# Optimization experiments

Hardware: AMD Instinct MI355X
Metric: run time of the kernel (lower is better)

## Reference

```python
import jax, jax.numpy as jnp
import numpy as np

INPUT_DIM = 1024
HIDDEN_DIM = 128
TEMPERATURE = 1.0
TOPK = 10  # hard-coded k in the original forward


def setup_inputs() -> dict:
    key = jax.random.key(0)
    ks = jax.random.split(key, 7)
    B, N = 8, 50000
    s_in = 1.0 / np.sqrt(INPUT_DIM)
    s_h = 1.0 / np.sqrt(HIDDEN_DIM)
    return {
        "x": jax.random.normal(ks[0], (B, N, INPUT_DIM), dtype=jnp.float32),
        # torch Linear weight is [out,in]; we store transposed [in,out] for x @ W
        "Wv": jax.random.uniform(ks[1], (INPUT_DIM, HIDDEN_DIM), jnp.float32, -s_in, s_in),
        "bv": jax.random.uniform(ks[2], (HIDDEN_DIM,), jnp.float32, -s_in, s_in),
        "Wu": jax.random.uniform(ks[3], (INPUT_DIM, HIDDEN_DIM), jnp.float32, -s_in, s_in),
        "bu": jax.random.uniform(ks[4], (HIDDEN_DIM,), jnp.float32, -s_in, s_in),
        "Ww": jax.random.uniform(ks[5], (HIDDEN_DIM, 1), jnp.float32, -s_h, s_h),
        "bw": jax.random.uniform(ks[6], (1,), jnp.float32, -s_h, s_h),
    }


def reference(x, Wv, bv, Wu, bu, Ww, bw):
    # x: [B, N, D]. Dropout is identity in eval mode.
    def per_bag(xi):  # xi: [N, D]
        A_V = jnp.tanh(xi @ Wv + bv)              # [N, H]
        A_U = jax.nn.sigmoid(xi @ Wu + bu)        # [N, H] (gated attention)
        A = A_V * A_U
        scores = ((A @ Ww) + bw)[:, 0] / TEMPERATURE  # [N]
        _, top_idx = jax.lax.top_k(scores, TOPK)
        _, tail_idx = jax.lax.top_k(-scores, TOPK)
        idx = jnp.concatenate([top_idx, tail_idx])     # [2k]
        w = jax.nn.softmax(scores[idx])                # softmax over truncated set
        Z = w @ xi[idx]                                # [D]
        # dense analogue of the per-instance attention list (None -> 0)
        atten = jnp.zeros_like(scores).at[idx].set(w)  # [N]
        return Z, atten

    Z, atten = jax.vmap(per_bag)(x)  # Z: [B, D], atten: [B, N]
    return Z, atten
```

## Files before the change

kernel.cpp:

```cpp
#include <hip/hip_runtime.h>
#include <math.h>
#include <float.h>

#define INPUT_DIM 1024
#define HIDDEN 128
#define KSEL 10
#define KC 12

#define BM 64
#define BK 64
#define KT (INPUT_DIM / BK)
#define STH 512
#define NSEL1 32

typedef short short8 __attribute__((ext_vector_type(8)));
typedef float f32x4 __attribute__((ext_vector_type(4)));

static __device__ __forceinline__ unsigned short f2bf(float f) {
    union { float f; unsigned u; } v; v.f = f;
    unsigned r = v.u + 0x7FFF + ((v.u >> 16) & 1);
    return (unsigned short)(r >> 16);
}
static __device__ __forceinline__ float fast_tanh(float a) {
    float e = __expf(2.0f * a);
    return 1.0f - 2.0f / (e + 1.0f);
}
static __device__ __forceinline__ float fast_sigmoid(float a) {
    return 1.0f / (1.0f + __expf(-a));
}

__global__ __launch_bounds__(64) void repack_kernel(
    const float* __restrict__ Wv, const float* __restrict__ Wu,
    unsigned short* __restrict__ wp_hi)
{
    int bid = blockIdx.x;
    int l = threadIdx.x;
    int pc = (bid & 15) * 16 + (l & 15);
    int h = pc >> 1;
    const float* src = (pc & 1) ? Wu : Wv;
    int kbase = (bid >> 4) * 32 + (l >> 4) * 8;
    size_t off = ((size_t)bid * 64 + l) * 8;
    #pragma unroll
    for (int e = 0; e < 8; ++e)
        wp_hi[off + e] = f2bf(src[(size_t)(kbase + e) * HIDDEN + h]);
}

__global__ __launch_bounds__(STH) void scores_kernel(
    const float* __restrict__ x, const unsigned short* __restrict__ wp,
    const float* __restrict__ bv, const float* __restrict__ bu,
    const float* __restrict__ Ww, const float* __restrict__ bw,
    float* __restrict__ scores, float* __restrict__ atten, int N)
{
    __shared__ __align__(16) unsigned short xs[4][BM * BK];
    __shared__ float partial[8][BM];

    const int tid = threadIdx.x;
    const int l = tid & 63;
    const int w = tid >> 6;
    const int b = blockIdx.y;
    const int i0 = blockIdx.x * BM;
    const float* xb = x + (size_t)b * N * INPUT_DIM;

    const float* gpx = xb + (size_t)min(i0 + w * 8 + (l >> 3), N - 1) * INPUT_DIM
                          + (l & 7) * 8;
    const int xwidx = (w * 8 + (l >> 3)) * BK + (((l & 7) ^ (l >> 3)) * 8);

    f32x4 acc[4][2];
    #pragma unroll
    for (int m = 0; m < 4; ++m)
        #pragma unroll
        for (int n = 0; n < 2; ++n)
            acc[m][n] = (f32x4){0.f, 0.f, 0.f, 0.f};

#define XLOAD(XA, XB, T) do { \
        const float* _p = gpx + (size_t)min((T), KT - 1) * BK; \
        XA = *(const float4*)_p; \
        XB = *(const float4*)(_p + 4); \
    } while (0)

#define XWRITE(XA, XB, SLOT) do { \
        unsigned p0, p1, p2, p3; \
        asm("v_cvt_pk_bf16_f32 %0, %1, %2" : "=v"(p0) : "v"(XA.x), "v"(XA.y)); \
        asm("v_cvt_pk_bf16_f32 %0, %1, %2" : "=v"(p1) : "v"(XA.z), "v"(XA.w)); \
        asm("v_cvt_pk_bf16_f32 %0, %1, %2" : "=v"(p2) : "v"(XB.x), "v"(XB.y)); \
        asm("v_cvt_pk_bf16_f32 %0, %1, %2" : "=v"(p3) : "v"(XB.z), "v"(XB.w)); \
        *(uint4*)(&xs[(SLOT)][xwidx]) = make_uint4(p0, p1, p2, p3); \
    } while (0)

#define BLOAD(BH, KT_) do { \
        int _ktc = min((KT_), KT - 1); \
        _Pragma("unroll") \
        for (int ks = 0; ks < 2; ++ks) \
            _Pragma("unroll") \
            for (int n = 0; n < 2; ++n) { \
                unsigned boff = (unsigned)(((((_ktc) * 2 + ks) * 16 + w * 2 + n) * 64 + l) * 8); \
                BH[ks][n] = *(const short8*)(wp + boff); \
            } \
    } while (0)

#define MFMA_KT(SLOT, BH) do { \
        __builtin_amdgcn_s_setprio(1); \
        _Pragma("unroll") \
        for (int ks = 0; ks < 2; ++ks) \
            _Pragma("unroll") \
            for (int m = 0; m < 4; ++m) { \
                int rowt = m * 16 + (l & 15); \
                int chunk = (ks * 4 + (l >> 4)) ^ (l & 7); \
                short8 a = *(const short8*)(&xs[(SLOT)][rowt * BK + chunk * 8]); \
                _Pragma("unroll") \
                for (int n = 0; n < 2; ++n) \
                    acc[m][n] = __builtin_amdgcn_mfma_f32_16x16x32_bf16(a, BH[ks][n], acc[m][n], 0, 0, 0); \
            } \
        __builtin_amdgcn_s_setprio(0); \
    } while (0)

#define LGKM_BARRIER() do { \
        asm volatile("s_waitcnt lgkmcnt(0)" ::: "memory"); \
        __builtin_amdgcn_s_barrier(); \
    } while (0)

    float4 xA0, xA1, xB0, xB1;
    short8 bhA[2][2], bhB[2][2];

    XLOAD(xA0, xA1, 0);
    BLOAD(bhA, 0);
    XWRITE(xA0, xA1, 0);
    XLOAD(xA0, xA1, 1);
    XLOAD(xB0, xB1, 2);
    BLOAD(bhB, 1);
    LGKM_BARRIER();

    for (int j = 0; j < KT / 4; ++j) {
        #pragma unroll
        for (int i = 0; i < 4; ++i) {
            const int kt = j * 4 + i;
            if ((i & 1) == 0) {
                MFMA_KT(i, bhA);
                __builtin_amdgcn_sched_barrier(0);
                XWRITE(xA0, xA1, (i + 1) & 3);
                BLOAD(bhA, kt + 2);
                XLOAD(xA0, xA1, kt + 3);
                __builtin_amdgcn_sched_barrier(0);
                LGKM_BARRIER();
            } else {
                MFMA_KT(i, bhB);
                __builtin_amdgcn_sched_barrier(0);
                XWRITE(xB0, xB1, (i + 1) & 3);
                BLOAD(bhB, kt + 2);
                XLOAD(xB0, xB1, kt + 3);
                __builtin_amdgcn_sched_barrier(0);
                LGKM_BARRIER();
            }
        }
    }

#undef XLOAD
#undef XWRITE
#undef BLOAD
#undef MFMA_KT
#undef LGKM_BARRIER

    float bvv[2], buu[2], www[2];
    #pragma unroll
    for (int n = 0; n < 2; ++n) {
        int h = (w * 32 + n * 16 + (l & 15)) >> 1;
        bvv[n] = bv[h]; buu[n] = bu[h]; www[n] = Ww[h];
    }
    const bool isV = ((l & 1) == 0);

    #pragma unroll
    for (int m = 0; m < 4; ++m) {
        float cs[4] = {0.f, 0.f, 0.f, 0.f};
        #pragma unroll
        for (int n = 0; n < 2; ++n) {
            #pragma unroll
            for (int r = 0; r < 4; ++r) {
                float v = acc[m][n][r];
                float u = __shfl_xor(v, 1, 64);
                if (isV)
                    cs[r] += fast_tanh(v + bvv[n]) * fast_sigmoid(u + buu[n]) * www[n];
            }
        }
        #pragma unroll
        for (int r = 0; r < 4; ++r) {
            #pragma unroll
            for (int off = 1; off < 16; off <<= 1)
                cs[r] += __shfl_xor(cs[r], off, 64);
        }
        if ((l & 15) == 0) {
            #pragma unroll
            for (int r = 0; r < 4; ++r)
                partial[w][m * 16 + (l >> 4) * 4 + r] = cs[r];
        }
    }
    __syncthreads();

    if (tid < BM) {
        int gi2 = i0 + tid;
        if (gi2 < N) {
            float s = bw[0];
            #pragma unroll
            for (int ww2 = 0; ww2 < 8; ++ww2) s += partial[ww2][tid];
            scores[(size_t)b * N + gi2] = s;
            atten[(size_t)b * N + gi2] = 0.0f;
        }
    }
}

__global__ __launch_bounds__(64) void select1_kernel(
    const float* __restrict__ scores, float* __restrict__ cv, int* __restrict__ ci,
    int N, int CH)
{
    const int r = blockIdx.x, b = blockIdx.y;
    const int tid = threadIdx.x;
    const float* s = scores + (size_t)b * N;
    const int start = r * CH;
    const int end = min(N, start + CH);

    float tv[KC]; int ti[KC];
    float lv[KC]; int li[KC];
    #pragma unroll
    for (int j = 0; j < KC; ++j) { tv[j] = -FLT_MAX; ti[j] = -1; lv[j] = FLT_MAX; li[j] = -1; }

    for (int i = start + tid; i < end; i += 64) {
        float v = s[i];
        if (v > tv[KC-1]) {
            #pragma unroll
            for (int j = KC-1; j >= 1; --j) {
                if (v > tv[j-1])      { tv[j] = tv[j-1]; ti[j] = ti[j-1]; }
                else if (v > tv[j])   { tv[j] = v;       ti[j] = i;       }
            }
            if (v > tv[0]) { tv[0] = v; ti[0] = i; }
        }
        if (v < lv[KC-1]) {
            #pragma unroll
            for (int j = KC-1; j >= 1; --j) {
                if (v < lv[j-1])      { lv[j] = lv[j-1]; li[j] = li[j-1]; }
                else if (v < lv[j])   { lv[j] = v;       li[j] = i;       }
            }
            if (v < lv[0]) { lv[0] = v; li[0] = i; }
        }
    }

    size_t base = ((size_t)b * NSEL1 + r) * 2 * KC;
    for (int rd = 0; rd < KC; ++rd) {
        float v = tv[0]; int who = tid;
        #pragma unroll
        for (int off = 32; off > 0; off >>= 1) {
            float ov = __shfl_down(v, off, 64);
            int ow = __shfl_down(who, off, 64);
            if (ov > v) { v = ov; who = ow; }
        }
        int bwho = __shfl(who, 0, 64);
        if (tid == bwho) {
            cv[base + rd] = tv[0]; ci[base + rd] = ti[0];
            #pragma unroll
            for (int j = 0; j < KC-1; ++j) { tv[j] = tv[j+1]; ti[j] = ti[j+1]; }
            tv[KC-1] = -FLT_MAX;
        }
    }
    for (int rd = 0; rd < KC; ++rd) {
        float v = lv[0]; int who = tid;
        #pragma unroll
        for (int off = 32; off > 0; off >>= 1) {
            float ov = __shfl_down(v, off, 64);
            int ow = __shfl_down(who, off, 64);
            if (ov < v) { v = ov; who = ow; }
        }
        int bwho = __shfl(who, 0, 64);
        if (tid == bwho) {
            cv[base + KC + rd] = lv[0]; ci[base + KC + rd] = li[0];
            #pragma unroll
            for (int j = 0; j < KC-1; ++j) { lv[j] = lv[j+1]; li[j] = li[j+1]; }
            lv[KC-1] = FLT_MAX;
        }
    }
}

__global__ __launch_bounds__(64) void select2_kernel(
    const float* __restrict__ cv, const int* __restrict__ ci,
    int* __restrict__ cand_idx)
{
    const int b = blockIdx.x;
    const int tid = threadIdx.x;

    float tv[KC]; int ti[KC];
    float lv[KC]; int li[KC];
    #pragma unroll
    for (int j = 0; j < KC; ++j) { tv[j] = -FLT_MAX; ti[j] = -1; lv[j] = FLT_MAX; li[j] = -1; }

    for (int c = tid; c < NSEL1 * KC; c += 64) {
        int rr = c / KC, jj = c % KC;
        size_t base = ((size_t)b * NSEL1 + rr) * 2 * KC;
        {
            float v = cv[base + jj]; int idx = ci[base + jj];
            if (v > tv[KC-1]) {
                #pragma unroll
                for (int j = KC-1; j >= 1; --j) {
                    if (v > tv[j-1])      { tv[j] = tv[j-1]; ti[j] = ti[j-1]; }
                    else if (v > tv[j])   { tv[j] = v;       ti[j] = idx;     }
                }
                if (v > tv[0]) { tv[0] = v; ti[0] = idx; }
            }
        }
        {
            float v = cv[base + KC + jj]; int idx = ci[base + KC + jj];
            if (v < lv[KC-1]) {
                #pragma unroll
                for (int j = KC-1; j >= 1; --j) {
                    if (v < lv[j-1])      { lv[j] = lv[j-1]; li[j] = li[j-1]; }
                    else if (v < lv[j])   { lv[j] = v;       li[j] = idx;     }
                }
                if (v < lv[0]) { lv[0] = v; li[0] = idx; }
            }
        }
    }

    for (int rd = 0; rd < KC; ++rd) {
        float v = tv[0]; int who = tid;
        #pragma unroll
        for (int off = 32; off > 0; off >>= 1) {
            float ov = __shfl_down(v, off, 64);
            int ow = __shfl_down(who, off, 64);
            if (ov > v) { v = ov; who = ow; }
        }
        int bwho = __shfl(who, 0, 64);
        if (tid == bwho) {
            cand_idx[b * 2 * KC + rd] = ti[0];
            #pragma unroll
            for (int j = 0; j < KC-1; ++j) { tv[j] = tv[j+1]; ti[j] = ti[j+1]; }
            tv[KC-1] = -FLT_MAX;
        }
    }
    for (int rd = 0; rd < KC; ++rd) {
        float v = lv[0]; int who = tid;
        #pragma unroll
        for (int off = 32; off > 0; off >>= 1) {
            float ov = __shfl_down(v, off, 64);
            int ow = __shfl_down(who, off, 64);
            if (ov < v) { v = ov; who = ow; }
        }
        int bwho = __shfl(who, 0, 64);
        if (tid == bwho) {
            cand_idx[b * 2 * KC + KC + rd] = li[0];
            #pragma unroll
            for (int j = 0; j < KC-1; ++j) { lv[j] = lv[j+1]; li[j] = li[j+1]; }
            lv[KC-1] = FLT_MAX;
        }
    }
}

__global__ __launch_bounds__(256) void rescore_kernel(
    const float* __restrict__ x,
    const float* __restrict__ Wv, const float* __restrict__ bv,
    const float* __restrict__ Wu, const float* __restrict__ bu,
    const float* __restrict__ Ww, const float* __restrict__ bw,
    const int* __restrict__ cand_idx, float* __restrict__ cand_score, int N)
{
    const int j = blockIdx.x, b = blockIdx.y;
    const int tid = threadIdx.x;
    __shared__ float xsr[INPUT_DIM];
    __shared__ float sp[4];

    int idx = cand_idx[b * 2 * KC + j];
    const float* xr = x + ((size_t)b * N + idx) * INPUT_DIM;
    *(float4*)(&xsr[tid * 4]) = *(const float4*)(&xr[tid * 4]);
    __syncthreads();

    const int h = tid >> 1;
    const int isU = tid & 1;
    const float* W = isU ? Wu : Wv;
    float s = 0.f;
    #pragma unroll 8
    for (int k = 0; k < INPUT_DIM; ++k)
        s = fmaf(xsr[k], W[(size_t)k * HIDDEN + h], s);

    float other = __shfl_xor(s, 1, 64);
    float g = 0.f;
    if (!isU) {
        float vv = tanhf(s + bv[h]);
        float uu = 1.0f / (1.0f + expf(-(other + bu[h])));
        g = vv * uu * Ww[h];
    }
    #pragma unroll
    for (int off = 1; off < 64; off <<= 1) g += __shfl_xor(g, off, 64);
    if ((tid & 63) == 0) sp[tid >> 6] = g;
    __syncthreads();
    if (tid == 0)
        cand_score[b * 2 * KC + j] = sp[0] + sp[1] + sp[2] + sp[3] + bw[0];
}

__global__ __launch_bounds__(256) void final_kernel(
    const float* __restrict__ x, const int* __restrict__ cand_idx,
    const float* __restrict__ cand_score,
    float* __restrict__ atten, float* __restrict__ Z, int N)
{
    const int b = blockIdx.x;
    const int tid = threadIdx.x;
    __shared__ int fidx[2 * KSEL];
    __shared__ float fw[2 * KSEL];

    if (tid == 0) {
        float cs[2 * KC]; int ciX[2 * KC]; bool used[2 * KC];
        #pragma unroll
        for (int j2 = 0; j2 < 2 * KC; ++j2) {
            cs[j2] = cand_score[b * 2 * KC + j2];
            ciX[j2] = cand_idx[b * 2 * KC + j2];
            used[j2] = false;
        }
        float fs[2 * KSEL];
        for (int r = 0; r < KSEL; ++r) {
            int best = -1; float bvv = -FLT_MAX;
            for (int j2 = 0; j2 < KC; ++j2)
                if (!used[j2] && cs[j2] > bvv) { bvv = cs[j2]; best = j2; }
            used[best] = true; fidx[r] = ciX[best]; fs[r] = bvv;
        }
        for (int r = 0; r < KSEL; ++r) {
            int best = -1; float bvv = FLT_MAX;
            for (int j2 = KC; j2 < 2 * KC; ++j2)
                if (!used[j2] && cs[j2] < bvv) { bvv = cs[j2]; best = j2; }
            used[best] = true; fidx[KSEL + r] = ciX[best]; fs[KSEL + r] = bvv;
        }
        float m = -FLT_MAX;
        for (int j2 = 0; j2 < 2 * KSEL; ++j2) m = fmaxf(m, fs[j2]);
        float e[2 * KSEL], sum = 0.f;
        for (int j2 = 0; j2 < 2 * KSEL; ++j2) { e[j2] = expf(fs[j2] - m); sum += e[j2]; }
        float inv = 1.0f / sum;
        for (int j2 = 0; j2 < 2 * KSEL; ++j2) {
            fw[j2] = e[j2] * inv;
            atten[(size_t)b * N + fidx[j2]] = fw[j2];
        }
    }
    __syncthreads();

    float4 acc = make_float4(0.f, 0.f, 0.f, 0.f);
    #pragma unroll
    for (int j2 = 0; j2 < 2 * KSEL; ++j2) {
        int idx = fidx[j2];
        float wgt = fw[j2];
        const float4* xr = (const float4*)(x + ((size_t)b * N + idx) * INPUT_DIM);
        float4 v = xr[tid];
        acc.x = fmaf(wgt, v.x, acc.x);
        acc.y = fmaf(wgt, v.y, acc.y);
        acc.z = fmaf(wgt, v.z, acc.z);
        acc.w = fmaf(wgt, v.w, acc.w);
    }
    ((float4*)(Z + (size_t)b * INPUT_DIM))[tid] = acc;
}

extern "C" void kernel_launch(void* const* d_in, const int* in_sizes, int n_in,
                              void* d_out, int out_size, void* d_ws, size_t ws_size,
                              hipStream_t stream)
{
    const float* x  = (const float*)d_in[0];
    const float* Wv = (const float*)d_in[1];
    const float* bv = (const float*)d_in[2];
    const float* Wu = (const float*)d_in[3];
    const float* bu = (const float*)d_in[4];
    const float* Ww = (const float*)d_in[5];
    const float* bw = (const float*)d_in[6];

    const int B = 8;
    const int N = in_sizes[0] / (B * INPUT_DIM);

    float* Z = (float*)d_out;
    float* atten = (float*)d_out + (size_t)B * INPUT_DIM;

    char* p = (char*)d_ws;
    float* scores = (float*)p;                  p += (size_t)B * N * sizeof(float);
    unsigned short* wp = (unsigned short*)p;    p += (size_t)INPUT_DIM * 256 * sizeof(unsigned short);
    float* cand_v = (float*)p;                  p += (size_t)B * NSEL1 * 2 * KC * sizeof(float);
    int* cand_i = (int*)p;                      p += (size_t)B * NSEL1 * 2 * KC * sizeof(int);
    int* cand_idx = (int*)p;                    p += (size_t)B * 2 * KC * sizeof(int);
    float* cand_score = (float*)p;

    repack_kernel<<<512, 64, 0, stream>>>(Wv, Wu, wp);

    dim3 g1((N + BM - 1) / BM, B);
    scores_kernel<<<g1, STH, 0, stream>>>(x, wp, bv, bu, Ww, bw, scores, atten, N);

    int CH = (N + NSEL1 - 1) / NSEL1;
    dim3 g2(NSEL1, B);
    select1_kernel<<<g2, 64, 0, stream>>>(scores, cand_v, cand_i, N, CH);
    select2_kernel<<<B, 64, 0, stream>>>(cand_v, cand_i, cand_idx);

    dim3 g3(2 * KC, B);
    rescore_kernel<<<g3, 256, 0, stream>>>(x, Wv, bv, Wu, bu, Ww, bw, cand_idx, cand_score, N);
    final_kernel<<<B, 256, 0, stream>>>(x, cand_idx, cand_score, atten, Z, N);
}
```

Before: 658.4 us.

## Use 4 waves per block with 64-column N tiles per wave in scores GEMM

The scores kernel drops from 8 to 4 waves per block. Each wave now covers 64 of the 256 packed output columns, holds a 4x4 accumulator grid, and loads two x rows per thread per K-step. The weight fragments are now loaded just in time before each MFMA step rather than double-buffered two K-tiles ahead. This reuses each LDS A-fragment read across more MFMAs and cuts the partial-sum reduction, but raises register pressure and exposes the global B-load latency right before the MFMAs.

```diff
diff --git a/kernel.cpp b/kernel.cpp
--- a/kernel.cpp
+++ b/kernel.cpp
@@ -10,7 +10,7 @@
 #define BM 64
 #define BK 64
 #define KT (INPUT_DIM / BK)
-#define STH 512
+#define STH 256
 #define NSEL1 32
 
 typedef short short8 __attribute__((ext_vector_type(8)));
@@ -52,7 +52,7 @@
     float* __restrict__ scores, float* __restrict__ atten, int N)
 {
     __shared__ __align__(16) unsigned short xs[4][BM * BK];
-    __shared__ float partial[8][BM];
+    __shared__ float partial[4][BM];
 
     const int tid = threadIdx.x;
     const int l = tid & 63;
@@ -61,44 +61,51 @@
     const int i0 = blockIdx.x * BM;
     const float* xb = x + (size_t)b * N * INPUT_DIM;
 
-    const float* gpx = xb + (size_t)min(i0 + w * 8 + (l >> 3), N - 1) * INPUT_DIM
-                          + (l & 7) * 8;
-    const int xwidx = (w * 8 + (l >> 3)) * BK + (((l & 7) ^ (l >> 3)) * 8);
-
-    f32x4 acc[4][2];
+    const float* gp0 = xb + (size_t)min(i0 + w * 16 + (l >> 3), N - 1) * INPUT_DIM + (l & 7) * 8;
+    const float* gp1 = xb + (size_t)min(i0 + w * 16 + 8 + (l >> 3), N - 1) * INPUT_DIM + (l & 7) * 8;
+    const int xw0 = (w * 16 + (l >> 3)) * BK + (((l & 7) ^ (l >> 3)) * 8);
+    const int xw1 = (w * 16 + 8 + (l >> 3)) * BK + (((l & 7) ^ (l >> 3)) * 8);
+
+    f32x4 acc[4][4];
     #pragma unroll
     for (int m = 0; m < 4; ++m)
         #pragma unroll
-        for (int n = 0; n < 2; ++n)
+        for (int n = 0; n < 4; ++n)
             acc[m][n] = (f32x4){0.f, 0.f, 0.f, 0.f};
 
-#define XLOAD(XA, XB, T) do { \
-        const float* _p = gpx + (size_t)min((T), KT - 1) * BK; \
-        XA = *(const float4*)_p; \
-        XB = *(const float4*)(_p + 4); \
+#define XLOAD(X0, X1, X2, X3, T) do { \
+        const size_t _o = (size_t)min((T), KT - 1) * BK; \
+        X0 = *(const float4*)(gp0 + _o); \
+        X1 = *(const float4*)(gp0 + _o + 4); \
+        X2 = *(const float4*)(gp1 + _o); \
+        X3 = *(const float4*)(gp1 + _o + 4); \
     } while (0)
 
-#define XWRITE(XA, XB, SLOT) do { \
-        unsigned p0, p1, p2, p3; \
-        asm("v_cvt_pk_bf16_f32 %0, %1, %2" : "=v"(p0) : "v"(XA.x), "v"(XA.y)); \
-        asm("v_cvt_pk_bf16_f32 %0, %1, %2" : "=v"(p1) : "v"(XA.z), "v"(XA.w)); \
-        asm("v_cvt_pk_bf16_f32 %0, %1, %2" : "=v"(p2) : "v"(XB.x), "v"(XB.y)); \
-        asm("v_cvt_pk_bf16_f32 %0, %1, %2" : "=v"(p3) : "v"(XB.z), "v"(XB.w)); \
-        *(uint4*)(&xs[(SLOT)][xwidx]) = make_uint4(p0, p1, p2, p3); \
+#define XWRITE(X0, X1, X2, X3, SLOT) do { \
+        unsigned p0, p1, p2, p3, q0, q1, q2, q3; \
+        asm("v_cvt_pk_bf16_f32 %0, %1, %2" : "=v"(p0) : "v"(X0.x), "v"(X0.y)); \
+        asm("v_cvt_pk_bf16_f32 %0, %1, %2" : "=v"(p1) : "v"(X0.z), "v"(X0.w)); \
+        asm("v_cvt_pk_bf16_f32 %0, %1, %2" : "=v"(p2) : "v"(X1.x), "v"(X1.y)); \
+        asm("v_cvt_pk_bf16_f32 %0, %1, %2" : "=v"(p3) : "v"(X1.z), "v"(X1.w)); \
+        asm("v_cvt_pk_bf16_f32 %0, %1, %2" : "=v"(q0) : "v"(X2.x), "v"(X2.y)); \
+        asm("v_cvt_pk_bf16_f32 %0, %1, %2" : "=v"(q1) : "v"(X2.z), "v"(X2.w)); \
+        asm("v_cvt_pk_bf16_f32 %0, %1, %2" : "=v"(q2) : "v"(X3.x), "v"(X3.y)); \
+        asm("v_cvt_pk_bf16_f32 %0, %1, %2" : "=v"(q3) : "v"(X3.z), "v"(X3.w)); \
+        *(uint4*)(&xs[(SLOT)][xw0]) = make_uint4(p0, p1, p2, p3); \
+        *(uint4*)(&xs[(SLOT)][xw1]) = make_uint4(q0, q1, q2, q3); \
     } while (0)
 
-#define BLOAD(BH, KT_) do { \
-        int _ktc = min((KT_), KT - 1); \
+#define BLOAD(KT_) do { \
         _Pragma("unroll") \
         for (int ks = 0; ks < 2; ++ks) \
             _Pragma("unroll") \
-            for (int n = 0; n < 2; ++n) { \
-                unsigned boff = (unsigned)(((((_ktc) * 2 + ks) * 16 + w * 2 + n) * 64 + l) * 8); \
-                BH[ks][n] = *(const short8*)(wp + boff); \
+            for (int n = 0; n < 4; ++n) { \
+                unsigned boff = (unsigned)(((((KT_) * 2 + ks) * 16 + w * 4 + n) * 64 + l) * 8); \
+                bh[ks][n] = *(const short8*)(wp + boff); \
             } \
     } while (0)
 
-#define MFMA_KT(SLOT, BH) do { \
+#define MFMA_KT(SLOT) do { \
         __builtin_amdgcn_s_setprio(1); \
         _Pragma("unroll") \
         for (int ks = 0; ks < 2; ++ks) \
@@ -108,8 +115,8 @@
                 int chunk = (ks * 4 + (l >> 4)) ^ (l & 7); \
                 short8 a = *(const short8*)(&xs[(SLOT)][rowt * BK + chunk * 8]); \
                 _Pragma("unroll") \
-                for (int n = 0; n < 2; ++n) \
-                    acc[m][n] = __builtin_amdgcn_mfma_f32_16x16x32_bf16(a, BH[ks][n], acc[m][n], 0, 0, 0); \
+                for (int n = 0; n < 4; ++n) \
+                    acc[m][n] = __builtin_amdgcn_mfma_f32_16x16x32_bf16(a, bh[ks][n], acc[m][n], 0, 0, 0); \
             } \
         __builtin_amdgcn_s_setprio(0); \
     } while (0)
@@ -119,38 +126,31 @@
         __builtin_amdgcn_s_barrier(); \
     } while (0)
 
-    float4 xA0, xA1, xB0, xB1;
-    short8 bhA[2][2], bhB[2][2];
-
-    XLOAD(xA0, xA1, 0);
-    BLOAD(bhA, 0);
-    XWRITE(xA0, xA1, 0);
-    XLOAD(xA0, xA1, 1);
-    XLOAD(xB0, xB1, 2);
-    BLOAD(bhB, 1);
+    short8 bh[2][4];
+    float4 a0, a1, a2, a3, c0, c1, c2, c3;
+
+    XLOAD(a0, a1, a2, a3, 0);
+    XWRITE(a0, a1, a2, a3, 0);
+    XLOAD(a0, a1, a2, a3, 1);
+    XLOAD(c0, c1, c2, c3, 2);
     LGKM_BARRIER();
 
     for (int j = 0; j < KT / 4; ++j) {
         #pragma unroll
-        for (int i = 0; i < 4; ++i) {
-            const int kt = j * 4 + i;
-            if ((i & 1) == 0) {
-                MFMA_KT(i, bhA);
-                __builtin_amdgcn_sched_barrier(0);
-                XWRITE(xA0, xA1, (i + 1) & 3);
-                BLOAD(bhA, kt + 2);
-                XLOAD(xA0, xA1, kt + 3);
-                __builtin_amdgcn_sched_barrier(0);
-                LGKM_BARRIER();
+        for (int ii = 0; ii < 4; ++ii) {
+            const int kt = j * 4 + ii;
+            BLOAD(kt);
+            MFMA_KT(ii);
+            __builtin_amdgcn_sched_barrier(0);
+            if ((ii & 1) == 0) {
+                XWRITE(a0, a1, a2, a3, (ii + 1) & 3);
+                XLOAD(a0, a1, a2, a3, kt + 3);
             } else {
-                MFMA_KT(i, bhB);
-                __builtin_amdgcn_sched_barrier(0);
-                XWRITE(xB0, xB1, (i + 1) & 3);
-                BLOAD(bhB, kt + 2);
-                XLOAD(xB0, xB1, kt + 3);
-                __builtin_amdgcn_sched_barrier(0);
-                LGKM_BARRIER();
-            }
+                XWRITE(c0, c1, c2, c3, (ii + 1) & 3);
+                XLOAD(c0, c1, c2, c3, kt + 3);
+            }
+            __builtin_amdgcn_sched_barrier(0);
+            LGKM_BARRIER();
         }
     }
 
@@ -160,10 +160,10 @@
 #undef MFMA_KT
 #undef LGKM_BARRIER
 
-    float bvv[2], buu[2], www[2];
-    #pragma unroll
-    for (int n = 0; n < 2; ++n) {
-        int h = (w * 32 + n * 16 + (l & 15)) >> 1;
+    float bvv[4], buu[4], www[4];
+    #pragma unroll
+    for (int n = 0; n < 4; ++n) {
+        int h = (w * 64 + n * 16 + (l & 15)) >> 1;
         bvv[n] = bv[h]; buu[n] = bu[h]; www[n] = Ww[h];
     }
     const bool isV = ((l & 1) == 0);
@@ -172,7 +172,7 @@
     for (int m = 0; m < 4; ++m) {
         float cs[4] = {0.f, 0.f, 0.f, 0.f};
         #pragma unroll
-        for (int n = 0; n < 2; ++n) {
+        for (int n = 0; n < 4; ++n) {
             #pragma unroll
             for (int r = 0; r < 4; ++r) {
                 float v = acc[m][n][r];
@@ -198,9 +198,8 @@
     if (tid < BM) {
         int gi2 = i0 + tid;
         if (gi2 < N) {
-            float s = bw[0];
-            #pragma unroll
-            for (int ww2 = 0; ww2 < 8; ++ww2) s += partial[ww2][tid];
+            float s = bw[0] + partial[0][tid] + partial[1][tid]
+                            + partial[2][tid] + partial[3][tid];
             scores[(size_t)b * N + gi2] = s;
             atten[(size_t)b * N + gi2] = 0.0f;
         }
```

Result: faster. 549.6 us (-16.5%).
